# Optimization experiments

Hardware: AMD Instinct MI355X
Metric: run time of the kernel (lower is better)

The kernel has to match this reference:

```python
import jax, jax.numpy as jnp
import numpy as np

N_QUBITS = 14
LATENT = 14
DEPTH = 4
BATCH = 256
DIM = 1 << N_QUBITS  # 16384 amplitudes

# PennyLane convention: wire 0 is the most-significant bit of the flat state index.
_idx = np.arange(DIM)
_bits = (_idx[None, :] >> (N_QUBITS - 1 - np.arange(N_QUBITS)[:, None])) & 1  # [n_qubits, DIM]
_parity = np.sum(_bits[:-1] * _bits[1:], axis=0) % 2  # adjacent-pair CZ chain parity
CZ_SIGNS = jnp.asarray(1.0 - 2.0 * _parity, dtype=jnp.complex64)  # [DIM]
Z_SIGNS = jnp.asarray(1 - 2 * _bits[:LATENT], dtype=jnp.float32)  # [LATENT, DIM]


def _rx(t):
    c = jnp.cos(0.5 * t) + 0j
    s = -1j * jnp.sin(0.5 * t)
    m = jnp.stack([jnp.stack([c, s], -1), jnp.stack([s, c], -1)], -2)
    return m.astype(jnp.complex64)


def _ry(t):
    c = jnp.cos(0.5 * t)
    s = jnp.sin(0.5 * t)
    m = jnp.stack([jnp.stack([c, -s], -1), jnp.stack([s, c], -1)], -2)
    return m.astype(jnp.complex64)


def _rz(t):
    e = jnp.exp(-0.5j * t.astype(jnp.complex64))
    z = jnp.zeros_like(e)
    m = jnp.stack([jnp.stack([e, z], -1), jnp.stack([z, jnp.conj(e)], -1)], -2)
    return m.astype(jnp.complex64)


def _apply_1q(state, mat, wire):
    # state: [B, DIM]; mat: [2,2] (shared) or [B,2,2] (per-sample)
    B = state.shape[0]
    left = 1 << wire
    right = 1 << (N_QUBITS - wire - 1)
    st = state.reshape(B, left, 2, right)
    if mat.ndim == 3:
        st = jnp.einsum('bij,bajc->baic', mat, st)
    else:
        st = jnp.einsum('ij,bajc->baic', mat, st)
    return st.reshape(B, DIM)


def setup_inputs() -> dict:
    key = jax.random.key(0)
    k1, k2, k3, k4 = jax.random.split(key, 4)
    conditioning = jax.random.normal(k1, (BATCH, LATENT), dtype=jnp.float32)
    lim = 1.0 / np.sqrt(LATENT)
    W_enc = jax.random.uniform(k2, (N_QUBITS, LATENT), jnp.float32, -lim, lim)
    b_enc = jax.random.uniform(k3, (N_QUBITS,), jnp.float32, -lim, lim)
    # TorchLayer default init: U(0, 2*pi)
    weights = jax.random.uniform(k4, (DEPTH, N_QUBITS, 3), jnp.float32, 0.0, 2.0 * np.pi)
    return {"conditioning": conditioning, "W_enc": W_enc, "b_enc": b_enc, "weights": weights}


def reference(conditioning, W_enc, b_enc, weights):
    # encode: Linear + SiLU -> per-wire rotation angles [B, n_qubits]
    emb = conditioning @ W_enc.T + b_enc
    emb = emb * jax.nn.sigmoid(emb)
    B = emb.shape[0]

    state = jnp.zeros((B, DIM), jnp.complex64).at[:, 0].set(1.0)

    # angle encoding: RX(v) then RY(v) on each wire (per-sample gates)
    for w in range(N_QUBITS):
        v = emb[:, w]
        U = jnp.einsum('bij,bjk->bik', _ry(v), _rx(v))  # [B,2,2]
        state = _apply_1q(state, U, w)

    # variational layers: RZ, RX, RY per wire (shared gates), then CZ chain
    for d in range(DEPTH):
        for w in range(N_QUBITS):
            p = weights[d, w]
            U = _ry(p[2]) @ _rx(p[1]) @ _rz(p[0])  # [2,2]
            state = _apply_1q(state, U, w)
        state = state * CZ_SIGNS  # all adjacent CZs fused into one diagonal

    probs = state.real ** 2 + state.imag ** 2  # [B, DIM]
    latent = probs @ Z_SIGNS.T  # <Z_w> for w in range(LATENT) -> [B, LATENT]

    # F.layer_norm over last dim, no affine params
    mu = jnp.mean(latent, axis=-1, keepdims=True)
    var = jnp.var(latent, axis=-1, keepdims=True)
    return (latent - mu) / jnp.sqrt(var + 1e-5)
```

## Files before the change

kernel.cpp:

```cpp
#include <hip/hip_runtime.h>
#include <math.h>

#define NQ    14
#define DIM   16384
#define DEPTH 4

typedef __attribute__((ext_vector_type(2))) float f2;
typedef __attribute__((ext_vector_type(4))) float f4;

__device__ __forceinline__ f2 cmul(f2 a, f2 b) {
    return (f2){a.x*b.x - a.y*b.y, a.x*b.y + a.y*b.x};
}
__device__ __forceinline__ f2 cmac2(f2 x, f2 u, f2 us, f2 y, f2 v, f2 vs) {
    f2 r = x.xx * u;
    r += x.yy * us;
    r += y.xx * v;
    r += y.yy * vs;
    return r;
}

__device__ __forceinline__ float czsgn(int e) {
    return (__popc(e & (e >> 1)) & 1) ? -1.0f : 1.0f;
}


template<int CTRL>
__device__ __forceinline__ f2 dpp2(f2 v) {
    union U { f2 f; int i[2]; } u, r;
    u.f = v;
    r.i[0] = __builtin_amdgcn_update_dpp(0, u.i[0], CTRL, 0xF, 0xF, true);
    r.i[1] = __builtin_amdgcn_update_dpp(0, u.i[1], CTRL, 0xF, 0xF, true);
    return r.f;
}
__device__ __forceinline__ f2 swzx4(f2 v) {
    union U { f2 f; int i[2]; } u, r;
    u.f = v;
    r.i[0] = __builtin_amdgcn_ds_swizzle(u.i[0], 0x101F);
    r.i[1] = __builtin_amdgcn_ds_swizzle(u.i[1], 0x101F);
    return r.f;
}
template<int XB> __device__ __forceinline__ f2 lxchg(f2 v);
template<> __device__ __forceinline__ f2 lxchg<1>(f2 v) { return dpp2<0xB1>(v); }
template<> __device__ __forceinline__ f2 lxchg<2>(f2 v) { return dpp2<0x4E>(v); }
template<> __device__ __forceinline__ f2 lxchg<4>(f2 v) { return swzx4(v); }
template<> __device__ __forceinline__ f2 lxchg<8>(f2 v) { return dpp2<0x128>(v); }

template<int MASK>
__device__ __forceinline__ void reg_gate(f2 a[16], const f4* G) {
    f4 g0 = G[0], g1 = G[1], g2 = G[2], g3 = G[3];
    #pragma unroll
    for (int l = 0; l < 16; ++l) {
        if (l & MASK) continue;
        const int j = l | MASK;
        f2 x = a[l], y = a[j];
        a[l] = cmac2(x, g0.xy, g0.zw, y, g1.xy, g1.zw);
        a[j] = cmac2(x, g2.xy, g2.zw, y, g3.xy, g3.zw);
    }
}

template<int XB>
__device__ __forceinline__ void lane_gate(f2 a[16], const f4* G, int t) {
    const bool hi = (t & XB) != 0;
    f4 c1 = G[hi ? 3 : 0];
    f4 c2 = G[hi ? 2 : 1];
    #pragma unroll
    for (int l = 0; l < 16; ++l) {
        f2 p = lxchg<XB>(a[l]);
        a[l] = cmac2(a[l], c1.xy, c1.zw, p, c2.xy, c2.zw);
    }
}

template<bool MULSIGN>
__device__ __forceinline__ void sweepA(f2* st, const f4 (*gl)[4], int t)
{
    f2 a[16];
    #pragma unroll
    for (int l = 0; l < 16; ++l) a[l] = st[t + (l << 10)];
    if (MULSIGN) {
        const int T = ((t & 15) << 6) | (t >> 4);
        const int pT = __popc(T & (T >> 1)) & 1;
        const float F0 = pT ? -1.f : 1.f;
        const float F1 = (pT ^ ((t >> 3) & 1)) ? -1.f : 1.f;
        #pragma unroll
        for (int l = 0; l < 16; ++l) {
            float s = (l & 1) ? F1 : F0;
            if (__popc(l & (l >> 1)) & 1) s = -s;
            a[l] *= s;
        }
    }
    reg_gate<8>(a, gl[0]);
    reg_gate<4>(a, gl[1]);
    reg_gate<2>(a, gl[2]);
    reg_gate<1>(a, gl[3]);
    lane_gate<8>(a, gl[4], t);
    lane_gate<4>(a, gl[5], t);
    lane_gate<2>(a, gl[6], t);
    lane_gate<1>(a, gl[7], t);
    #pragma unroll
    for (int l = 0; l < 16; ++l) st[t + (l << 10)] = a[l];
}

__device__ __forceinline__ int baseB(int t) {
    return ((t >> 2) & 15) | ((t & 3) << 4) | ((t >> 6) << 10);
}

__device__ __forceinline__ void sweepB(f2* st, const f4 (*gl)[4], int t)
{
    const int mb = baseB(t);
    f2 a[16];
    #pragma unroll
    for (int l = 0; l < 16; ++l) a[l] = st[mb + (l << 6)];
    reg_gate<8>(a, gl[8]);
    reg_gate<4>(a, gl[9]);
    reg_gate<2>(a, gl[10]);
    reg_gate<1>(a, gl[11]);
    lane_gate<2>(a, gl[12], t);
    lane_gate<1>(a, gl[13], t);
    #pragma unroll
    for (int l = 0; l < 16; ++l) st[mb + (l << 6)] = a[l];
}

__device__ __forceinline__ void sweepB_final(f2* st, const f4 (*gl)[4], int t,
        float& SU, float& Q8, float& Q9, float& Q10, float& Q11)
{
    const int mb = baseB(t);
    f2 a[16];
    #pragma unroll
    for (int l = 0; l < 16; ++l) a[l] = st[mb + (l << 6)];
    reg_gate<8>(a, gl[8]);
    reg_gate<4>(a, gl[9]);
    reg_gate<2>(a, gl[10]);
    reg_gate<1>(a, gl[11]);
    lane_gate<2>(a, gl[12], t);
    lane_gate<1>(a, gl[13], t);
    SU = Q8 = Q9 = Q10 = Q11 = 0.f;
    #pragma unroll
    for (int l = 0; l < 16; ++l) {
        float p = a[l].x*a[l].x + a[l].y*a[l].y;
        SU  += p;
        Q8  += (l & 8) ? -p : p;
        Q9  += (l & 4) ? -p : p;
        Q10 += (l & 2) ? -p : p;
        Q11 += (l & 1) ? -p : p;
    }
}

__global__ __launch_bounds__(1024)
void qlg_kernel(const float* __restrict__ cond,
                const float* __restrict__ Wenc,
                const float* __restrict__ benc,
                const float* __restrict__ wts,
                float* __restrict__ out)
{
    __shared__ f2 st[DIM];
    __shared__ f4 gates[DEPTH][NQ][4];
    __shared__ f2 qv[NQ][2];
    __shared__ f2 Phi[128];
    __shared__ f2 Plo[128];
    __shared__ float embS[NQ];
    __shared__ float wred[16][NQ];
    __shared__ float lat[NQ];

    const int b = blockIdx.x;
    const int t = threadIdx.x;

    if (t < NQ) {
        float s = benc[t];
        #pragma unroll
        for (int k = 0; k < NQ; ++k) s += cond[b*NQ + k] * Wenc[t*NQ + k];
        embS[t] = s / (1.0f + __expf(-s));
    }
    if (t >= 64 && t < 64 + DEPTH*NQ) {
        const int gi = t - 64;
        const int d = gi / NQ, w = gi % NQ;
        const float p0 = wts[(d*NQ + w)*3 + 0];
        const float p1 = wts[(d*NQ + w)*3 + 1];
        const float p2 = wts[(d*NQ + w)*3 + 2];
        float s0, c0, s1, c1, s2, c2;
        sincosf(0.5f*p0, &s0, &c0);
        sincosf(0.5f*p1, &s1, &c1);
        sincosf(0.5f*p2, &s2, &c2);
        f2 e0  = (f2){c0, -s0};
        f2 e0c = (f2){c0,  s0};
        f2 is1 = (f2){0.f, -s1};
        f2 m00 = c1 * e0;
        f2 m01 = cmul(is1, e0c);
        f2 m10 = cmul(is1, e0);
        f2 m11 = c1 * e0c;
        f2 u00 = c2*m00 - s2*m10;
        f2 u01 = c2*m01 - s2*m11;
        f2 u10 = s2*m00 + c2*m10;
        f2 u11 = s2*m01 + c2*m11;
        gates[d][w][0] = (f4){u00.x, u00.y, -u00.y, u00.x};
        gates[d][w][1] = (f4){u01.x, u01.y, -u01.y, u01.x};
        gates[d][w][2] = (f4){u10.x, u10.y, -u10.y, u10.x};
        gates[d][w][3] = (f4){u11.x, u11.y, -u11.y, u11.x};
    }
    __syncthreads();

    if (t < NQ) {
        float v = embS[t];
        float s, c;
        sincosf(0.5f*v, &s, &c);
        f2 a0 = (f2){c*c,  s*s};
        f2 a1 = (f2){s*c, -s*c};
        f2 u00 = gates[0][t][0].xy, u01 = gates[0][t][1].xy;
        f2 u10 = gates[0][t][2].xy, u11 = gates[0][t][3].xy;
        qv[t][0] = cmul(u00, a0) + cmul(u01, a1);
        qv[t][1] = cmul(u10, a0) + cmul(u11, a1);
    }
    __syncthreads();

    if (t < 128) {
        f2 p = qv[0][(t >> 6) & 1];
        #pragma unroll
        for (int w = 1; w <= 6; ++w) p = cmul(p, qv[w][(t >> (6 - w)) & 1]);
        Phi[t] = p;
    } else if (t < 256) {
        const int j = t - 128;
        f2 p = qv[7][(j >> 6) & 1];
        #pragma unroll
        for (int w = 8; w <= 13; ++w) p = cmul(p, qv[w][(j >> (13 - w)) & 1]);
        Plo[j] = p;
    }
    __syncthreads();

    #pragma unroll
    for (int l = 0; l < 16; ++l) {
        const int e = (l << 10) | ((t & 15) << 6) | (t >> 4);
        f2 v = cmul(Phi[e >> 7], Plo[e & 127]);
        st[t + (l << 10)] = v * czsgn(e);
    }
    __syncthreads();

    sweepA<false>(st, gates[1], t); __syncthreads();
    sweepB(st, gates[1], t);        __syncthreads();
    sweepA<true>(st, gates[2], t);  __syncthreads();
    sweepB(st, gates[2], t);        __syncthreads();
    sweepA<true>(st, gates[3], t);  __syncthreads();
    float SU, Q8, Q9, Q10, Q11;
    sweepB_final(st, gates[3], t, SU, Q8, Q9, Q10, Q11);

    {
        const int lane = t & 63, wv = t >> 6;
        #pragma unroll
        for (int w = 0; w < NQ; ++w) {
            float v;
            if      (w == 8)  v = Q8;
            else if (w == 9)  v = Q9;
            else if (w == 10) v = Q10;
            else if (w == 11) v = Q11;
            else if (w <= 7)  v = ((t >> (9 - w)) & 1) ? -SU : SU;
            else              v = ((t >> (13 - w)) & 1) ? -SU : SU;
            #pragma unroll
            for (int off = 32; off > 0; off >>= 1) v += __shfl_down(v, off, 64);
            if (lane == 0) wred[wv][w] = v;
        }
    }
    __syncthreads();
    if (t < NQ) {
        float s = 0.f;
        #pragma unroll
        for (int k = 0; k < 16; ++k) s += wred[k][t];
        lat[t] = s;
    }
    __syncthreads();
    if (t < NQ) {
        float mu = 0.f;
        #pragma unroll
        for (int k = 0; k < NQ; ++k) mu += lat[k];
        mu *= (1.0f / NQ);
        float var = 0.f;
        #pragma unroll
        for (int k = 0; k < NQ; ++k) { float dv = lat[k] - mu; var += dv*dv; }
        var *= (1.0f / NQ);
        out[b*NQ + t] = (lat[t] - mu) * rsqrtf(var + 1e-5f);
    }
}

extern "C" void kernel_launch(void* const* d_in, const int* in_sizes, int n_in,
                              void* d_out, int out_size, void* d_ws, size_t ws_size,
                              hipStream_t stream)
{
    (void)n_in; (void)d_ws; (void)ws_size; (void)out_size;
    const float* cond = (const float*)d_in[0];
    const float* Wenc = (const float*)d_in[1];
    const float* benc = (const float*)d_in[2];
    const float* wts  = (const float*)d_in[3];
    float* out = (float*)d_out;
    const int B = in_sizes[0] / NQ;
    qlg_kernel<<<dim3(B), dim3(1024), 0, stream>>>(cond, Wenc, benc, wts, out);
}
```

Before: 98.46 us.

## Restructure state-vector sweeps to cut LDS round trips using wide lane exchanges

The qubit-to-register/lane mapping is reorganised so each thread handles 4 register qubits and 6 lane qubits, using swizzle and shfl_xor for lane distances 16 and 32. Several variational layers are fused across the CZ diagonal without going through shared memory, which reduces LDS store/load phases and barriers from about six to three. The initial product state is built directly in registers instead of being written to LDS first. The cost is more cross-lane exchanges, including slower shfl_xor for distance 32 and ds_swizzle for 16, plus more complex sign bookkeeping for the CZ phases.

```diff
diff --git a/kernel.cpp b/kernel.cpp
--- a/kernel.cpp
+++ b/kernel.cpp
@@ -17,10 +17,6 @@
     r += y.xx * v;
     r += y.yy * vs;
     return r;
-}
-
-__device__ __forceinline__ float czsgn(int e) {
-    return (__popc(e & (e >> 1)) & 1) ? -1.0f : 1.0f;
 }
 
 
@@ -32,18 +28,27 @@
     r.i[1] = __builtin_amdgcn_update_dpp(0, u.i[1], CTRL, 0xF, 0xF, true);
     return r.f;
 }
-__device__ __forceinline__ f2 swzx4(f2 v) {
+template<int PAT>
+__device__ __forceinline__ f2 swz2(f2 v) {
     union U { f2 f; int i[2]; } u, r;
     u.f = v;
-    r.i[0] = __builtin_amdgcn_ds_swizzle(u.i[0], 0x101F);
-    r.i[1] = __builtin_amdgcn_ds_swizzle(u.i[1], 0x101F);
+    r.i[0] = __builtin_amdgcn_ds_swizzle(u.i[0], PAT);
+    r.i[1] = __builtin_amdgcn_ds_swizzle(u.i[1], PAT);
     return r.f;
 }
 template<int XB> __device__ __forceinline__ f2 lxchg(f2 v);
-template<> __device__ __forceinline__ f2 lxchg<1>(f2 v) { return dpp2<0xB1>(v); }
-template<> __device__ __forceinline__ f2 lxchg<2>(f2 v) { return dpp2<0x4E>(v); }
-template<> __device__ __forceinline__ f2 lxchg<4>(f2 v) { return swzx4(v); }
-template<> __device__ __forceinline__ f2 lxchg<8>(f2 v) { return dpp2<0x128>(v); }
+template<> __device__ __forceinline__ f2 lxchg<1>(f2 v)  { return dpp2<0xB1>(v); }
+template<> __device__ __forceinline__ f2 lxchg<2>(f2 v)  { return dpp2<0x4E>(v); }
+template<> __device__ __forceinline__ f2 lxchg<4>(f2 v)  { return swz2<0x101F>(v); }
+template<> __device__ __forceinline__ f2 lxchg<8>(f2 v)  { return dpp2<0x128>(v); }
+template<> __device__ __forceinline__ f2 lxchg<16>(f2 v) { return swz2<0x401F>(v); }
+template<> __device__ __forceinline__ f2 lxchg<32>(f2 v) {
+    union U { f2 f; float s[2]; } u, r;
+    u.f = v;
+    r.s[0] = __shfl_xor(u.s[0], 32, 64);
+    r.s[1] = __shfl_xor(u.s[1], 32, 64);
+    return r.f;
+}
 
 template<int MASK>
 __device__ __forceinline__ void reg_gate(f2 a[16], const f4* G) {
@@ -70,78 +75,29 @@
     }
 }
 
-template<bool MULSIGN>
-__device__ __forceinline__ void sweepA(f2* st, const f4 (*gl)[4], int t)
-{
-    f2 a[16];
-    #pragma unroll
-    for (int l = 0; l < 16; ++l) a[l] = st[t + (l << 10)];
-    if (MULSIGN) {
-        const int T = ((t & 15) << 6) | (t >> 4);
-        const int pT = __popc(T & (T >> 1)) & 1;
-        const float F0 = pT ? -1.f : 1.f;
-        const float F1 = (pT ^ ((t >> 3) & 1)) ? -1.f : 1.f;
-        #pragma unroll
-        for (int l = 0; l < 16; ++l) {
-            float s = (l & 1) ? F1 : F0;
-            if (__popc(l & (l >> 1)) & 1) s = -s;
-            a[l] *= s;
-        }
-    }
-    reg_gate<8>(a, gl[0]);
-    reg_gate<4>(a, gl[1]);
-    reg_gate<2>(a, gl[2]);
-    reg_gate<1>(a, gl[3]);
-    lane_gate<8>(a, gl[4], t);
-    lane_gate<4>(a, gl[5], t);
-    lane_gate<2>(a, gl[6], t);
-    lane_gate<1>(a, gl[7], t);
-    #pragma unroll
-    for (int l = 0; l < 16; ++l) st[t + (l << 10)] = a[l];
-}
-
-__device__ __forceinline__ int baseB(int t) {
-    return ((t >> 2) & 15) | ((t & 3) << 4) | ((t >> 6) << 10);
-}
-
-__device__ __forceinline__ void sweepB(f2* st, const f4 (*gl)[4], int t)
-{
-    const int mb = baseB(t);
-    f2 a[16];
-    #pragma unroll
-    for (int l = 0; l < 16; ++l) a[l] = st[mb + (l << 6)];
-    reg_gate<8>(a, gl[8]);
-    reg_gate<4>(a, gl[9]);
-    reg_gate<2>(a, gl[10]);
-    reg_gate<1>(a, gl[11]);
-    lane_gate<2>(a, gl[12], t);
-    lane_gate<1>(a, gl[13], t);
-    #pragma unroll
-    for (int l = 0; l < 16; ++l) st[mb + (l << 6)] = a[l];
-}
-
-__device__ __forceinline__ void sweepB_final(f2* st, const f4 (*gl)[4], int t,
-        float& SU, float& Q8, float& Q9, float& Q10, float& Q11)
-{
-    const int mb = baseB(t);
-    f2 a[16];
-    #pragma unroll
-    for (int l = 0; l < 16; ++l) a[l] = st[mb + (l << 6)];
-    reg_gate<8>(a, gl[8]);
-    reg_gate<4>(a, gl[9]);
-    reg_gate<2>(a, gl[10]);
-    reg_gate<1>(a, gl[11]);
-    lane_gate<2>(a, gl[12], t);
-    lane_gate<1>(a, gl[13], t);
-    SU = Q8 = Q9 = Q10 = Q11 = 0.f;
+__device__ __forceinline__ void cz_M0(f2 a[16], int t) {
+    const int n = t & 63, w = t >> 6;
+    const int pT = (__popc(w & (w >> 1)) + __popc(n & (n >> 1)) + ((n & 1) & (w >> 3))) & 1;
+    const float F0 = pT ? -1.f : 1.f;
+    const float F1 = (pT ^ ((n >> 5) & 1)) ? -1.f : 1.f;
     #pragma unroll
     for (int l = 0; l < 16; ++l) {
-        float p = a[l].x*a[l].x + a[l].y*a[l].y;
-        SU  += p;
-        Q8  += (l & 8) ? -p : p;
-        Q9  += (l & 4) ? -p : p;
-        Q10 += (l & 2) ? -p : p;
-        Q11 += (l & 1) ? -p : p;
+        float s = (l & 1) ? F1 : F0;
+        if (__popc(l & (l >> 1)) & 1) s = -s;
+        a[l] *= s;
+    }
+}
+
+__device__ __forceinline__ void cz_M1(f2 a[16], int t) {
+    const int n = t & 63, w = t >> 6;
+    const int pT = (__popc(w & (w >> 1)) + __popc(n & (n >> 1)) + ((w & 1) & (n >> 5))) & 1;
+    const float F0 = pT ? -1.f : 1.f;
+    const float F1 = (pT ^ (n & 1)) ? -1.f : 1.f;
+    #pragma unroll
+    for (int l = 0; l < 16; ++l) {
+        float s = (l & 8) ? F1 : F0;
+        if (__popc(l & (l >> 1)) & 1) s = -s;
+        a[l] *= s;
     }
 }
 
@@ -163,6 +119,8 @@
 
     const int b = blockIdx.x;
     const int t = threadIdx.x;
+    const int n = t & 63, w = t >> 6;
+    const int bM1 = n | (w << 10);
 
     if (t < NQ) {
         float s = benc[t];
@@ -172,10 +130,10 @@
     }
     if (t >= 64 && t < 64 + DEPTH*NQ) {
         const int gi = t - 64;
-        const int d = gi / NQ, w = gi % NQ;
-        const float p0 = wts[(d*NQ + w)*3 + 0];
-        const float p1 = wts[(d*NQ + w)*3 + 1];
-        const float p2 = wts[(d*NQ + w)*3 + 2];
+        const int d = gi / NQ, ww = gi % NQ;
+        const float p0 = wts[(d*NQ + ww)*3 + 0];
+        const float p1 = wts[(d*NQ + ww)*3 + 1];
+        const float p2 = wts[(d*NQ + ww)*3 + 2];
         float s0, c0, s1, c1, s2, c2;
         sincosf(0.5f*p0, &s0, &c0);
         sincosf(0.5f*p1, &s1, &c1);
@@ -191,10 +149,10 @@
         f2 u01 = c2*m01 - s2*m11;
         f2 u10 = s2*m00 + c2*m10;
         f2 u11 = s2*m01 + c2*m11;
-        gates[d][w][0] = (f4){u00.x, u00.y, -u00.y, u00.x};
-        gates[d][w][1] = (f4){u01.x, u01.y, -u01.y, u01.x};
-        gates[d][w][2] = (f4){u10.x, u10.y, -u10.y, u10.x};
-        gates[d][w][3] = (f4){u11.x, u11.y, -u11.y, u11.x};
+        gates[d][ww][0] = (f4){u00.x, u00.y, -u00.y, u00.x};
+        gates[d][ww][1] = (f4){u01.x, u01.y, -u01.y, u01.x};
+        gates[d][ww][2] = (f4){u10.x, u10.y, -u10.y, u10.x};
+        gates[d][ww][3] = (f4){u11.x, u11.y, -u11.y, u11.x};
     }
     __syncthreads();
 
@@ -214,47 +172,132 @@
     if (t < 128) {
         f2 p = qv[0][(t >> 6) & 1];
         #pragma unroll
-        for (int w = 1; w <= 6; ++w) p = cmul(p, qv[w][(t >> (6 - w)) & 1]);
+        for (int ww = 1; ww <= 6; ++ww) p = cmul(p, qv[ww][(t >> (6 - ww)) & 1]);
         Phi[t] = p;
     } else if (t < 256) {
         const int j = t - 128;
         f2 p = qv[7][(j >> 6) & 1];
         #pragma unroll
-        for (int w = 8; w <= 13; ++w) p = cmul(p, qv[w][(j >> (13 - w)) & 1]);
+        for (int ww = 8; ww <= 13; ++ww) p = cmul(p, qv[ww][(j >> (13 - ww)) & 1]);
         Plo[j] = p;
     }
     __syncthreads();
 
-    #pragma unroll
-    for (int l = 0; l < 16; ++l) {
-        const int e = (l << 10) | ((t & 15) << 6) | (t >> 4);
-        f2 v = cmul(Phi[e >> 7], Plo[e & 127]);
-        st[t + (l << 10)] = v * czsgn(e);
-    }
-    __syncthreads();
-
-    sweepA<false>(st, gates[1], t); __syncthreads();
-    sweepB(st, gates[1], t);        __syncthreads();
-    sweepA<true>(st, gates[2], t);  __syncthreads();
-    sweepB(st, gates[2], t);        __syncthreads();
-    sweepA<true>(st, gates[3], t);  __syncthreads();
-    float SU, Q8, Q9, Q10, Q11;
-    sweepB_final(st, gates[3], t, SU, Q8, Q9, Q10, Q11);
+    f2 a[16];
+    {
+        f2 plo = Plo[((n & 7) << 4) | w];
+        #pragma unroll
+        for (int l = 0; l < 16; ++l)
+            a[l] = cmul(Phi[(l << 3) | (n >> 3)], plo);
+        cz_M0(a, t);
+    }
+
+    {
+        const f4 (*gl)[4] = gates[1];
+        reg_gate<8>(a, gl[0]);
+        reg_gate<4>(a, gl[1]);
+        reg_gate<2>(a, gl[2]);
+        reg_gate<1>(a, gl[3]);
+        lane_gate<32>(a, gl[4], t);
+        lane_gate<16>(a, gl[5], t);
+        lane_gate<8>(a, gl[6], t);
+        lane_gate<4>(a, gl[7], t);
+        lane_gate<2>(a, gl[8], t);
+        lane_gate<1>(a, gl[9], t);
+    }
+
+    #pragma unroll
+    for (int l = 0; l < 16; ++l) st[t + (l << 10)] = a[l];
+    __syncthreads();
+    #pragma unroll
+    for (int l = 0; l < 16; ++l) a[l] = st[bM1 + (l << 6)];
+
+    {
+        const f4 (*gl1)[4] = gates[1];
+        reg_gate<8>(a, gl1[10]);
+        reg_gate<4>(a, gl1[11]);
+        reg_gate<2>(a, gl1[12]);
+        reg_gate<1>(a, gl1[13]);
+        cz_M1(a, t);
+        const f4 (*gl2)[4] = gates[2];
+        lane_gate<32>(a, gl2[4], t);
+        lane_gate<16>(a, gl2[5], t);
+        lane_gate<8>(a, gl2[6], t);
+        lane_gate<4>(a, gl2[7], t);
+        lane_gate<2>(a, gl2[8], t);
+        lane_gate<1>(a, gl2[9], t);
+        reg_gate<8>(a, gl2[10]);
+        reg_gate<4>(a, gl2[11]);
+        reg_gate<2>(a, gl2[12]);
+        reg_gate<1>(a, gl2[13]);
+    }
+
+    __syncthreads();
+    #pragma unroll
+    for (int l = 0; l < 16; ++l) st[bM1 + (l << 6)] = a[l];
+    __syncthreads();
+    #pragma unroll
+    for (int l = 0; l < 16; ++l) a[l] = st[t + (l << 10)];
+
+    {
+        const f4 (*gl2)[4] = gates[2];
+        reg_gate<8>(a, gl2[0]);
+        reg_gate<4>(a, gl2[1]);
+        reg_gate<2>(a, gl2[2]);
+        reg_gate<1>(a, gl2[3]);
+        cz_M0(a, t);
+        const f4 (*gl3)[4] = gates[3];
+        reg_gate<8>(a, gl3[0]);
+        reg_gate<4>(a, gl3[1]);
+        reg_gate<2>(a, gl3[2]);
+        reg_gate<1>(a, gl3[3]);
+        lane_gate<32>(a, gl3[4], t);
+        lane_gate<16>(a, gl3[5], t);
+        lane_gate<8>(a, gl3[6], t);
+        lane_gate<4>(a, gl3[7], t);
+        lane_gate<2>(a, gl3[8], t);
+        lane_gate<1>(a, gl3[9], t);
+    }
+
+    __syncthreads();
+    #pragma unroll
+    for (int l = 0; l < 16; ++l) st[t + (l << 10)] = a[l];
+    __syncthreads();
+    #pragma unroll
+    for (int l = 0; l < 16; ++l) a[l] = st[bM1 + (l << 6)];
+
+    float SU, Q10, Q11, Q12, Q13;
+    {
+        const f4 (*gl3)[4] = gates[3];
+        reg_gate<8>(a, gl3[10]);
+        reg_gate<4>(a, gl3[11]);
+        reg_gate<2>(a, gl3[12]);
+        reg_gate<1>(a, gl3[13]);
+        SU = Q10 = Q11 = Q12 = Q13 = 0.f;
+        #pragma unroll
+        for (int l = 0; l < 16; ++l) {
+            float p = a[l].x*a[l].x + a[l].y*a[l].y;
+            SU  += p;
+            Q10 += (l & 8) ? -p : p;
+            Q11 += (l & 4) ? -p : p;
+            Q12 += (l & 2) ? -p : p;
+            Q13 += (l & 1) ? -p : p;
+        }
+    }
 
     {
         const int lane = t & 63, wv = t >> 6;
         #pragma unroll
-        for (int w = 0; w < NQ; ++w) {
+        for (int ww = 0; ww < NQ; ++ww) {
             float v;
-            if      (w == 8)  v = Q8;
-            else if (w == 9)  v = Q9;
-            else if (w == 10) v = Q10;
-            else if (w == 11) v = Q11;
-            else if (w <= 7)  v = ((t >> (9 - w)) & 1) ? -SU : SU;
-            else              v = ((t >> (13 - w)) & 1) ? -SU : SU;
+            if      (ww == 10) v = Q10;
+            else if (ww == 11) v = Q11;
+            else if (ww == 12) v = Q12;
+            else if (ww == 13) v = Q13;
+            else               v = ((t >> (9 - ww)) & 1) ? -SU : SU;
             #pragma unroll
             for (int off = 32; off > 0; off >>= 1) v += __shfl_down(v, off, 64);
-            if (lane == 0) wred[wv][w] = v;
+            if (lane == 0) wred[wv][ww] = v;
         }
     }
     __syncthreads();
```

New measurement: 95.81 us. 2.7% less time.
